# Optimization experiments

Measured on AMD Instinct MI355X. Metric: run time of the kernel, lower is better.

Reference implementation:

```python
import jax, jax.numpy as jnp
import numpy as np
from jax import lax

K, HE, HD = 4, 96, 192  # kernel_size, hidden_enc, hidden_dec (HD == 2*HE required by z -> decoder hidden)

def _conv1d(x, W, b):
    y = lax.conv_general_dilated(x, W, (1,), 'VALID', dimension_numbers=('NCH', 'OIH', 'NCH'))
    return y + b[None, :, None]

def _maxpool1d(x, k):
    return lax.reduce_window(x, -jnp.inf, lax.max, (1, 1, k), (1, 1, k), 'VALID')

def _gru_scan(x, h0, Wi, Wh, bi, bh, emit):
    # x: (B, S, D); standard PyTorch GRU cell math
    xw = jnp.einsum('bsd,gd->sbg', x, Wi) + bi  # (S, B, 3H)
    def step(h, xw_t):
        xr, xz, xn = jnp.split(xw_t, 3, axis=-1)
        hr, hz, hn = jnp.split(h @ Wh.T + bh, 3, axis=-1)
        r = jax.nn.sigmoid(xr + hr)
        zg = jax.nn.sigmoid(xz + hz)
        n = jnp.tanh(xn + r * hn)
        h_new = (1.0 - zg) * n + zg * h
        return h_new, (h_new if emit else None)
    return lax.scan(step, h0, xw)

def _bigru(x, Wif, Whf, bif, bhf, Wib, Whb, bib, bhb, H):
    h0 = jnp.zeros((x.shape[0], H), x.dtype)
    _, of = _gru_scan(x, h0, Wif, Whf, bif, bhf, True)           # (S, B, H)
    _, ob = _gru_scan(x[:, ::-1], h0, Wib, Whb, bib, bhb, True)  # reverse direction
    return jnp.swapaxes(jnp.concatenate([of, ob[::-1]], axis=-1), 0, 1)  # (B, S, 2H)

def _forward(input, W_c1, b_c1, W_c2, b_c2, Wi_muf, Wh_muf, bi_muf, bh_muf, Wi_mub, Wh_mub, bi_mub, bh_mub, Wi_sgf, Wh_sgf, bi_sgf, bh_sgf, Wi_sgb, Wh_sgb, bi_sgb, bh_sgb, Wi_d, Wh_d, bi_d, bh_d, Wl, bl):
    T = input.shape[1]  # input: (B, T, T); input_dim == seq_len == T
    # Encoder: NodeConv (conv -> relu -> maxpool -> conv -> relu); dropout=0 -> identity
    h = jax.nn.relu(_conv1d(input, W_c1, b_c1))
    h = _maxpool1d(h, K)
    h = jax.nn.relu(_conv1d(h, W_c2, b_c2))  # (B, C, F)
    om = _bigru(h, Wi_muf, Wh_muf, bi_muf, bh_muf, Wi_mub, Wh_mub, bi_mub, bh_mub, HE)
    mu = jnp.concatenate([om[:, -1, :HE], om[:, 0, HE:]], axis=1)
    og = _bigru(h, Wi_sgf, Wh_sgf, bi_sgf, bh_sgf, Wi_sgb, Wh_sgb, bi_sgb, bh_sgb, HE)
    logvar = jnp.concatenate([og[:, -1, :HE], og[:, 0, HE:]], axis=1)
    eps = jax.random.normal(jax.random.key(42), mu.shape, mu.dtype)  # fixed-eps reparameterize
    z = mu + eps * jnp.exp(0.5 * logvar)  # (B, HD)
    # Decoder: leave-one-out per-timestep GRU recompute; hidden carried across outer steps
    base = jnp.arange(T - 1)
    def outer(h_c, i):
        idx = base + (base >= i).astype(base.dtype)  # indices skipping position i
        seq = jnp.take(input, idx, axis=1)           # (B, T-1, T)
        h_new, _ = _gru_scan(seq, h_c, Wi_d, Wh_d, bi_d, bh_d, False)
        return h_new, h_new @ Wl.T + bl
    _, outs = lax.scan(outer, z, jnp.arange(T))
    return jnp.swapaxes(outs, 0, 1), mu, logvar  # (B, T, T), (B, HD), (B, HD)

def setup_inputs():
    keys = iter(jax.random.split(jax.random.key(0), 40))
    def w(*shape):
        return jax.random.normal(next(keys), shape, jnp.float32) * 0.1
    B, D, C, F = 16, 96, 64, 20  # F = ((96-4+1)//4) - 4 + 1
    inp = {"input": jax.random.normal(next(keys), (B, D, D), jnp.float32)}
    inp["W_c1"], inp["b_c1"] = w(C, D, K), jnp.zeros((C,), jnp.float32)
    inp["W_c2"], inp["b_c2"] = w(C, C, K), jnp.zeros((C,), jnp.float32)
    for nm in ["muf", "mub", "sgf", "sgb"]:
        inp["Wi_" + nm] = w(3 * HE, F)
        inp["Wh_" + nm] = w(3 * HE, HE)
        inp["bi_" + nm] = jnp.zeros((3 * HE,), jnp.float32)
        inp["bh_" + nm] = jnp.zeros((3 * HE,), jnp.float32)
    inp["Wi_d"], inp["Wh_d"] = w(3 * HD, D), w(3 * HD, HD)
    inp["bi_d"], inp["bh_d"] = jnp.zeros((3 * HD,), jnp.float32), jnp.zeros((3 * HD,), jnp.float32)
    inp["Wl"], inp["bl"] = w(D, HD), jnp.zeros((D,), jnp.float32)
    return inp

def reference(input, W_c1, b_c1, W_c2, b_c2, Wi_muf, Wh_muf, bi_muf, bh_muf, Wi_mub, Wh_mub, bi_mub, bh_mub, Wi_sgf, Wh_sgf, bi_sgf, bh_sgf, Wi_sgb, Wh_sgb, bi_sgb, bh_sgb, Wi_d, Wh_d, bi_d, bh_d, Wl, bl):
    return _forward(input, W_c1, b_c1, W_c2, b_c2, Wi_muf, Wh_muf, bi_muf, bh_muf, Wi_mub, Wh_mub, bi_mub, bh_mub, Wi_sgf, Wh_sgf, bi_sgf, bh_sgf, Wi_sgb, Wh_sgb, bi_sgb, bh_sgb, Wi_d, Wh_d, bi_d, bh_d, Wl, bl)
```

## Files before the change

kernel.cpp:

```cpp
#include <hip/hip_runtime.h>
#include <math.h>
#include <stdint.h>


namespace {

constexpr int B  = 16;
constexpr int T  = 96;
constexpr int C  = 64;
constexpr int L1 = 93;
constexpr int LP = 23;
constexpr int F  = 20;
constexpr int HE = 96;
constexpr int GE = 288;
constexpr int HD = 192;
constexpr int GD = 576;
constexpr int SD = 95;

constexpr int WS_HENC = 0;
constexpr int WS_Z    = WS_HENC + B * C * F;
constexpr int WS_XW   = WS_Z + B * HD;
constexpr int WS_WHH  = WS_XW + B * T * GD;

constexpr int OUT_MU = B * T * T;
constexpr int OUT_LV = OUT_MU + B * HD;

typedef _Float16 half8 __attribute__((ext_vector_type(8)));
typedef float f32x4  __attribute__((ext_vector_type(4)));

constexpr float LOG2E  = 1.4426950408889634f;
constexpr float LOG2E2 = 2.8853900817779268f;

__device__ __forceinline__ float sigmf(float x) { return 1.0f / (1.0f + expf(-x)); }

__device__ __forceinline__ float fsig(float v) {
  float u = __builtin_amdgcn_exp2f(v * -LOG2E);
  return __builtin_amdgcn_rcpf(1.0f + u);
}
__device__ __forceinline__ float ftanh(float v) {
  float u = __builtin_amdgcn_exp2f(v * LOG2E2);
  return fmaf(-2.0f, __builtin_amdgcn_rcpf(1.0f + u), 1.0f);
}

__global__ __launch_bounds__(256) void enc_conv(
    const float* __restrict__ input, const float* __restrict__ Wc1,
    const float* __restrict__ bc1, const float* __restrict__ Wc2,
    const float* __restrict__ bc2, float* __restrict__ h_enc) {
  __shared__ float xin[T * T];
  __shared__ float y1[C * L1];
  const int b = blockIdx.x;
  for (int i = threadIdx.x; i < T * T; i += 256) xin[i] = input[b * T * T + i];
  __syncthreads();
  for (int idx = threadIdx.x; idx < C * L1; idx += 256) {
    const int o = idx / L1, t = idx - o * L1;
    const float* w = Wc1 + o * (T * 4);
    float acc = bc1[o];
#pragma unroll 8
    for (int i = 0; i < T; ++i) {
      float4 wv = *reinterpret_cast<const float4*>(w + i * 4);
      const float* xp = xin + i * T + t;
      acc = fmaf(wv.x, xp[0], acc);
      acc = fmaf(wv.y, xp[1], acc);
      acc = fmaf(wv.z, xp[2], acc);
      acc = fmaf(wv.w, xp[3], acc);
    }
    y1[idx] = fmaxf(acc, 0.0f);
  }
  __syncthreads();
  float* pl = xin;
  for (int idx = threadIdx.x; idx < C * LP; idx += 256) {
    const int o = idx / LP, t = idx - o * LP;
    const float* yp = y1 + o * L1 + 4 * t;
    pl[idx] = fmaxf(fmaxf(yp[0], yp[1]), fmaxf(yp[2], yp[3]));
  }
  __syncthreads();
  for (int idx = threadIdx.x; idx < C * F; idx += 256) {
    const int o = idx / F, t = idx - o * F;
    const float* w = Wc2 + o * (C * 4);
    float acc = bc2[o];
#pragma unroll 8
    for (int i = 0; i < C; ++i) {
      float4 wv = *reinterpret_cast<const float4*>(w + i * 4);
      const float* xp = pl + i * LP + t;
      acc = fmaf(wv.x, xp[0], acc);
      acc = fmaf(wv.y, xp[1], acc);
      acc = fmaf(wv.z, xp[2], acc);
      acc = fmaf(wv.w, xp[3], acc);
    }
    h_enc[b * (C * F) + idx] = fmaxf(acc, 0.0f);
  }
}

__global__ __launch_bounds__(320) void enc_gru(
    const float* __restrict__ h_enc,
    const float* __restrict__ Wi0, const float* __restrict__ Wh0,
    const float* __restrict__ bi0, const float* __restrict__ bh0,
    const float* __restrict__ Wi1, const float* __restrict__ Wh1,
    const float* __restrict__ bi1, const float* __restrict__ bh1,
    const float* __restrict__ Wi2, const float* __restrict__ Wh2,
    const float* __restrict__ bi2, const float* __restrict__ bh2,
    const float* __restrict__ Wi3, const float* __restrict__ Wh3,
    const float* __restrict__ bi3, const float* __restrict__ bh3,
    float* __restrict__ out) {
  const int chain = blockIdx.x >> 4;
  const int b = blockIdx.x & 15;
  const float *Wi, *Wh, *bi, *bh;
  if (chain == 0)      { Wi = Wi0; Wh = Wh0; bi = bi0; bh = bh0; }
  else if (chain == 1) { Wi = Wi1; Wh = Wh1; bi = bi1; bh = bh1; }
  else if (chain == 2) { Wi = Wi2; Wh = Wh2; bi = bi2; bh = bh2; }
  else                 { Wi = Wi3; Wh = Wh3; bi = bi3; bh = bh3; }
  const bool fwd = (chain & 1) == 0;
  const int off = ((chain >> 1) ? OUT_LV : OUT_MU) + b * HD + (fwd ? 0 : HE);

  __shared__ float xall[C * F];
  __shared__ float h[HE];
  __shared__ float gx[GE], ghs[GE];

  const int tid = threadIdx.x;
  for (int i = tid; i < C * F; i += 320) xall[i] = h_enc[b * (C * F) + i];
  if (tid < HE) h[tid] = 0.0f;

  float wi[F], wh[HE], big = 0.0f, bhg = 0.0f;
  if (tid < GE) {
#pragma unroll
    for (int d = 0; d < F; ++d) wi[d] = Wi[tid * F + d];
#pragma unroll
    for (int k = 0; k < HE; ++k) wh[k] = Wh[tid * HE + k];
    big = bi[tid];
    bhg = bh[tid];
  }
  __syncthreads();

  for (int s = 0; s < C; ++s) {
    const int se = fwd ? s : (C - 1 - s);
    if (tid < GE) {
      const float* xr = xall + se * F;
      float ax = big, ah = bhg;
#pragma unroll
      for (int d = 0; d < F; ++d) ax = fmaf(wi[d], xr[d], ax);
#pragma unroll
      for (int k = 0; k < HE; ++k) ah = fmaf(wh[k], h[k], ah);
      gx[tid] = ax;
      ghs[tid] = ah;
    }
    __syncthreads();
    if (tid < HE) {
      const float r  = sigmf(gx[tid] + ghs[tid]);
      const float zg = sigmf(gx[HE + tid] + ghs[HE + tid]);
      const float n  = tanhf(fmaf(r, ghs[2 * HE + tid], gx[2 * HE + tid]));
      h[tid] = fmaf(zg, h[tid] - n, n);
    }
    __syncthreads();
  }
  if (tid < HE) out[off + tid] = h[tid];
}

__device__ __forceinline__ uint32_t rotl32(uint32_t v, int d) {
  return (v << d) | (v >> (32 - d));
}

__device__ __forceinline__ float erfinv32(float x) {
  float w = -log1pf(-x * x);
  float p;
  if (w < 5.0f) {
    w -= 2.5f;
    p = 2.81022636e-08f;
    p = fmaf(p, w, 3.43273939e-07f);
    p = fmaf(p, w, -3.5233877e-06f);
    p = fmaf(p, w, -4.39150654e-06f);
    p = fmaf(p, w, 0.00021858087f);
    p = fmaf(p, w, -0.00125372503f);
    p = fmaf(p, w, -0.00417768164f);
    p = fmaf(p, w, 0.246640727f);
    p = fmaf(p, w, 1.50140941f);
  } else {
    w = sqrtf(w) - 3.0f;
    p = -0.000200214257f;
    p = fmaf(p, w, 0.000100950558f);
    p = fmaf(p, w, 0.00134934322f);
    p = fmaf(p, w, -0.00367342844f);
    p = fmaf(p, w, 0.00573950773f);
    p = fmaf(p, w, -0.0076224613f);
    p = fmaf(p, w, 0.00943887047f);
    p = fmaf(p, w, 1.00167406f);
    p = fmaf(p, w, 2.83297682f);
  }
  return p * x;
}

__global__ __launch_bounds__(256) void z_kernel(const float* __restrict__ dout,
                                                float* __restrict__ z) {
  const int p = blockIdx.x * 256 + threadIdx.x;
  if (p >= 1536) return;
  const uint32_t ks0 = 0u, ks1 = 42u;
  const uint32_t ks2 = 0x1BD11BDAu ^ ks0 ^ ks1;
  uint32_t x0 = (uint32_t)p + ks0;
  uint32_t x1 = (uint32_t)(p + 1536) + ks1;
  x0 += x1; x1 = rotl32(x1, 13) ^ x0;
  x0 += x1; x1 = rotl32(x1, 15) ^ x0;
  x0 += x1; x1 = rotl32(x1, 26) ^ x0;
  x0 += x1; x1 = rotl32(x1, 6)  ^ x0;
  x0 += ks1; x1 += ks2 + 1u;
  x0 += x1; x1 = rotl32(x1, 17) ^ x0;
  x0 += x1; x1 = rotl32(x1, 29) ^ x0;
  x0 += x1; x1 = rotl32(x1, 16) ^ x0;
  x0 += x1; x1 = rotl32(x1, 24) ^ x0;
  x0 += ks2; x1 += ks0 + 2u;
  x0 += x1; x1 = rotl32(x1, 13) ^ x0;
  x0 += x1; x1 = rotl32(x1, 15) ^ x0;
  x0 += x1; x1 = rotl32(x1, 26) ^ x0;
  x0 += x1; x1 = rotl32(x1, 6)  ^ x0;
  x0 += ks0; x1 += ks1 + 3u;
  x0 += x1; x1 = rotl32(x1, 17) ^ x0;
  x0 += x1; x1 = rotl32(x1, 29) ^ x0;
  x0 += x1; x1 = rotl32(x1, 16) ^ x0;
  x0 += x1; x1 = rotl32(x1, 24) ^ x0;
  x0 += ks1; x1 += ks2 + 4u;
  x0 += x1; x1 = rotl32(x1, 13) ^ x0;
  x0 += x1; x1 = rotl32(x1, 15) ^ x0;
  x0 += x1; x1 = rotl32(x1, 26) ^ x0;
  x0 += x1; x1 = rotl32(x1, 6)  ^ x0;
  x0 += ks2; x1 += ks0 + 5u;

  const float* mu = dout + OUT_MU;
  const float* lv = dout + OUT_LV;
  const float lo = -0.99999994f;
#pragma unroll
  for (int half = 0; half < 2; ++half) {
    const uint32_t bits = half ? x1 : x0;
    const int e = half ? (p + 1536) : p;
    const float f = __builtin_bit_cast(float, (bits >> 9) | 0x3F800000u) - 1.0f;
    const float u = fmaxf(lo, fmaf(f, 2.0f, lo));
    const float eps = 1.41421356f * erfinv32(u);
    z[e] = fmaf(eps, expf(0.5f * lv[e]), mu[e]);
  }
}

__global__ __launch_bounds__(192) void dec_xw(const float* __restrict__ input,
                                              const float* __restrict__ Wi,
                                              const float* __restrict__ bi,
                                              const float* __restrict__ bh,
                                              float* __restrict__ XW) {
  const int br = blockIdx.x;
  __shared__ float xrow[T];
  if (threadIdx.x < T) xrow[threadIdx.x] = input[br * T + threadIdx.x];
  __syncthreads();
  for (int g = threadIdx.x; g < GD; g += 192) {
    const float* w = Wi + g * T;
    float acc = bi[g] + (g < 2 * HD ? bh[g] : 0.0f);
#pragma unroll 8
    for (int d = 0; d < T; ++d) acc = fmaf(w[d], xrow[d], acc);
    XW[br * GD + g] = acc;
  }
}

__global__ __launch_bounds__(256) void wh_to_f16(const float* __restrict__ w,
                                                 _Float16* __restrict__ o) {
  const int i = blockIdx.x * 256 + threadIdx.x;
  if (i < GD * HD) o[i] = (_Float16)w[i];
}

__global__ __launch_bounds__(768, 3) void decoder(
    const float* __restrict__ XW, const _Float16* __restrict__ WhH,
    const float* __restrict__ bh, const float* __restrict__ z,
    const float* __restrict__ Wl, const float* __restrict__ bl,
    float* __restrict__ dout) {
  const int b = blockIdx.x;
  const int tid = threadIdx.x;
  const int lane = tid & 63;
  const int w = tid >> 6;
  const int col = lane & 15;
  const int g4 = lane >> 4;
  const int hidx = 16 * w + col;

  __shared__ alignas(16) _Float16 hb[2][256];
  __shared__ alignas(16) float hf[HD];

  half8 bR[6], bZ[6], bN[6];
#pragma unroll
  for (int kk = 0; kk < 6; ++kk) {
    const int ko = 32 * kk + 8 * g4;
    bR[kk] = *reinterpret_cast<const half8*>(WhH + hidx * HD + ko);
    bZ[kk] = *reinterpret_cast<const half8*>(WhH + (HD + hidx) * HD + ko);
    bN[kk] = *reinterpret_cast<const half8*>(WhH + (2 * HD + hidx) * HD + ko);
  }
  const float bhn = bh[2 * HD + hidx];

  float hold = z[b * HD + hidx];
  if (g4 == 0) hb[0][hidx] = (_Float16)hold;
  __syncthreads();

  const f32x4 kZero = {0.0f, 0.0f, 0.0f, 0.0f};
  const _Float16* hrd0 = &hb[0][8 * g4];
  _Float16* hwr0 = &hb[0][hidx];
  int cur = 0;
  const float* xwb = XW + b * T * GD;

  for (int i = 0; i < T; ++i) {
    for (int s = 0; s < SD; ++s) {
      const int rr = s + (s >= i ? 1 : 0);
      const float* xwrow = xwb + rr * GD;
      const float xr = xwrow[hidx];
      const float xz = xwrow[HD + hidx];
      const float xn = xwrow[2 * HD + hidx];

      const _Float16* hp = hrd0 + cur;
      half8 a[6];
#pragma unroll
      for (int kk = 0; kk < 6; ++kk)
        a[kk] = *reinterpret_cast<const half8*>(hp + 32 * kk);

      f32x4 aR = __builtin_amdgcn_mfma_f32_16x16x32_f16(a[0], bR[0], kZero, 0, 0, 0);
      f32x4 aZ = __builtin_amdgcn_mfma_f32_16x16x32_f16(a[0], bZ[0], kZero, 0, 0, 0);
      f32x4 aN = __builtin_amdgcn_mfma_f32_16x16x32_f16(a[0], bN[0], kZero, 0, 0, 0);
#pragma unroll
      for (int kk = 1; kk < 6; ++kk) {
        aR = __builtin_amdgcn_mfma_f32_16x16x32_f16(a[kk], bR[kk], aR, 0, 0, 0);
        aZ = __builtin_amdgcn_mfma_f32_16x16x32_f16(a[kk], bZ[kk], aZ, 0, 0, 0);
        aN = __builtin_amdgcn_mfma_f32_16x16x32_f16(a[kk], bN[kk], aN, 0, 0, 0);
      }
      const float r  = fsig(xr + aR[0]);
      const float zg = fsig(xz + aZ[0]);
      const float n  = ftanh(fmaf(r, aN[0] + bhn, xn));
      hold = fmaf(zg, hold - n, n);

      if (g4 == 0) {
        *(hwr0 + (cur ^ 256)) = (_Float16)hold;
        if (s == SD - 1) hf[hidx] = hold;
      }
      __syncthreads();
      cur ^= 256;
    }
    if (tid < T) {
      const float* wl = Wl + tid * HD;
      float acc = bl[tid];
#pragma unroll 8
      for (int k = 0; k < HD; ++k) acc = fmaf(wl[k], hf[k], acc);
      dout[(b * T + i) * T + tid] = acc;
    }
  }
}

}

extern "C" void kernel_launch(void* const* d_in, const int* in_sizes, int n_in,
                              void* d_out, int out_size, void* d_ws,
                              size_t ws_size, hipStream_t stream) {
  const float* input  = (const float*)d_in[0];
  const float* Wc1    = (const float*)d_in[1];
  const float* bc1    = (const float*)d_in[2];
  const float* Wc2    = (const float*)d_in[3];
  const float* bc2    = (const float*)d_in[4];
  const float* Wi_muf = (const float*)d_in[5];
  const float* Wh_muf = (const float*)d_in[6];
  const float* bi_muf = (const float*)d_in[7];
  const float* bh_muf = (const float*)d_in[8];
  const float* Wi_mub = (const float*)d_in[9];
  const float* Wh_mub = (const float*)d_in[10];
  const float* bi_mub = (const float*)d_in[11];
  const float* bh_mub = (const float*)d_in[12];
  const float* Wi_sgf = (const float*)d_in[13];
  const float* Wh_sgf = (const float*)d_in[14];
  const float* bi_sgf = (const float*)d_in[15];
  const float* bh_sgf = (const float*)d_in[16];
  const float* Wi_sgb = (const float*)d_in[17];
  const float* Wh_sgb = (const float*)d_in[18];
  const float* bi_sgb = (const float*)d_in[19];
  const float* bh_sgb = (const float*)d_in[20];
  const float* Wi_d   = (const float*)d_in[21];
  const float* Wh_d   = (const float*)d_in[22];
  const float* bi_d   = (const float*)d_in[23];
  const float* bh_d   = (const float*)d_in[24];
  const float* Wl     = (const float*)d_in[25];
  const float* bl     = (const float*)d_in[26];

  float* ws = (float*)d_ws;
  float* h_enc = ws + WS_HENC;
  float* zbuf  = ws + WS_Z;
  float* XW    = ws + WS_XW;
  _Float16* WhH = (_Float16*)(ws + WS_WHH);
  float* out = (float*)d_out;

  enc_conv<<<B, 256, 0, stream>>>(input, Wc1, bc1, Wc2, bc2, h_enc);
  enc_gru<<<64, 320, 0, stream>>>(h_enc, Wi_muf, Wh_muf, bi_muf, bh_muf,
                                  Wi_mub, Wh_mub, bi_mub, bh_mub,
                                  Wi_sgf, Wh_sgf, bi_sgf, bh_sgf,
                                  Wi_sgb, Wh_sgb, bi_sgb, bh_sgb, out);
  z_kernel<<<6, 256, 0, stream>>>(out, zbuf);
  dec_xw<<<B * T, 192, 0, stream>>>(input, Wi_d, bi_d, bh_d, XW);
  wh_to_f16<<<(GD * HD + 255) / 256, 256, 0, stream>>>(Wh_d, WhH);
  decoder<<<B, 768, 0, stream>>>(XW, WhH, bh_d, zbuf, Wl, bl, out);
}
```

Baseline: 6.373 ms.

## Prescale GRU gate weights by log2e and compute n-gate via fdot2

Folds the log2(e) and 2*log2(e) factors of the sigmoid and tanh into the precomputed input projections, the f16 recurrent weights and the n-gate bias, so the per-step activations skip one multiply each. It also replaces the third MFMA chain (n gate) with packed f16 dot products per lane, reduced across the four 16-lane groups with two cross-lane shuffles. The goal is to shorten the serial per-step critical path by moving work from the MFMA pipe to the VALU. The risk is that the shuffles and extra VALU instructions add latency of their own, and scaling weights before the f16 cast changes rounding slightly.

```diff
diff --git a/kernel.cpp b/kernel.cpp
--- a/kernel.cpp
+++ b/kernel.cpp
@@ -26,6 +26,7 @@
 constexpr int OUT_LV = OUT_MU + B * HD;
 
 typedef _Float16 half8 __attribute__((ext_vector_type(8)));
+typedef _Float16 half2v __attribute__((ext_vector_type(2)));
 typedef float f32x4  __attribute__((ext_vector_type(4)));
 
 constexpr float LOG2E  = 1.4426950408889634f;
@@ -33,13 +34,11 @@
 
 __device__ __forceinline__ float sigmf(float x) { return 1.0f / (1.0f + expf(-x)); }
 
-__device__ __forceinline__ float fsig(float v) {
-  float u = __builtin_amdgcn_exp2f(v * -LOG2E);
-  return __builtin_amdgcn_rcpf(1.0f + u);
-}
-__device__ __forceinline__ float ftanh(float v) {
-  float u = __builtin_amdgcn_exp2f(v * LOG2E2);
-  return fmaf(-2.0f, __builtin_amdgcn_rcpf(1.0f + u), 1.0f);
+__device__ __forceinline__ float fsig2(float xp) {
+  return __builtin_amdgcn_rcpf(1.0f + __builtin_amdgcn_exp2f(-xp));
+}
+__device__ __forceinline__ float ftanh2(float vp) {
+  return fmaf(-2.0f, __builtin_amdgcn_rcpf(1.0f + __builtin_amdgcn_exp2f(vp)), 1.0f);
 }
 
 __global__ __launch_bounds__(256) void enc_conv(
@@ -250,14 +249,15 @@
     float acc = bi[g] + (g < 2 * HD ? bh[g] : 0.0f);
 #pragma unroll 8
     for (int d = 0; d < T; ++d) acc = fmaf(w[d], xrow[d], acc);
-    XW[br * GD + g] = acc;
+    XW[br * GD + g] = acc * (g < 2 * HD ? LOG2E : LOG2E2);
   }
 }
 
 __global__ __launch_bounds__(256) void wh_to_f16(const float* __restrict__ w,
                                                  _Float16* __restrict__ o) {
   const int i = blockIdx.x * 256 + threadIdx.x;
-  if (i < GD * HD) o[i] = (_Float16)w[i];
+  if (i < GD * HD)
+    o[i] = (_Float16)(w[i] * (i < 2 * HD * HD ? LOG2E : LOG2E2));
 }
 
 __global__ __launch_bounds__(768, 3) void decoder(
@@ -284,7 +284,7 @@
     bZ[kk] = *reinterpret_cast<const half8*>(WhH + (HD + hidx) * HD + ko);
     bN[kk] = *reinterpret_cast<const half8*>(WhH + (2 * HD + hidx) * HD + ko);
   }
-  const float bhn = bh[2 * HD + hidx];
+  const float bhn = bh[2 * HD + hidx] * LOG2E2;
 
   float hold = z[b * HD + hidx];
   if (g4 == 0) hb[0][hidx] = (_Float16)hold;
@@ -312,16 +312,33 @@
 
       f32x4 aR = __builtin_amdgcn_mfma_f32_16x16x32_f16(a[0], bR[0], kZero, 0, 0, 0);
       f32x4 aZ = __builtin_amdgcn_mfma_f32_16x16x32_f16(a[0], bZ[0], kZero, 0, 0, 0);
-      f32x4 aN = __builtin_amdgcn_mfma_f32_16x16x32_f16(a[0], bN[0], kZero, 0, 0, 0);
 #pragma unroll
       for (int kk = 1; kk < 6; ++kk) {
         aR = __builtin_amdgcn_mfma_f32_16x16x32_f16(a[kk], bR[kk], aR, 0, 0, 0);
         aZ = __builtin_amdgcn_mfma_f32_16x16x32_f16(a[kk], bZ[kk], aZ, 0, 0, 0);
-        aN = __builtin_amdgcn_mfma_f32_16x16x32_f16(a[kk], bN[kk], aN, 0, 0, 0);
       }
-      const float r  = fsig(xr + aR[0]);
-      const float zg = fsig(xz + aZ[0]);
-      const float n  = ftanh(fmaf(r, aN[0] + bhn, xn));
+
+      float pn0 = 0.0f, pn1 = 0.0f;
+#pragma unroll
+      for (int kk = 0; kk < 6; ++kk) {
+        const uint4 au = __builtin_bit_cast(uint4, a[kk]);
+        const uint4 bu = __builtin_bit_cast(uint4, bN[kk]);
+        pn0 = __builtin_amdgcn_fdot2(__builtin_bit_cast(half2v, au.x),
+                                     __builtin_bit_cast(half2v, bu.x), pn0, false);
+        pn1 = __builtin_amdgcn_fdot2(__builtin_bit_cast(half2v, au.y),
+                                     __builtin_bit_cast(half2v, bu.y), pn1, false);
+        pn0 = __builtin_amdgcn_fdot2(__builtin_bit_cast(half2v, au.z),
+                                     __builtin_bit_cast(half2v, bu.z), pn0, false);
+        pn1 = __builtin_amdgcn_fdot2(__builtin_bit_cast(half2v, au.w),
+                                     __builtin_bit_cast(half2v, bu.w), pn1, false);
+      }
+      float pn = pn0 + pn1;
+      pn += __shfl_xor(pn, 16, 64);
+      pn += __shfl_xor(pn, 32, 64);
+
+      const float r  = fsig2(xr + aR[0]);
+      const float zg = fsig2(xz + aZ[0]);
+      const float n  = ftanh2(fmaf(r, pn + bhn, xn));
       hold = fmaf(zg, hold - n, n);
 
       if (g4 == 0) {
```

Result: slower. 7.836 ms (+22.9%).
